# Kernel tuning notes

Measured on AMD Instinct MI355X. Metric: run time of the kernel, lower is better.

The kernel has to match this reference:

```python
import jax, jax.numpy as jnp
import numpy as np

B, NQ, C = 2, 16384, 768
NH, NL, NP = 6, 1, 4
HW = 128
D = C // NH  # 128, deform_ratio = 1.0
EPS = 1e-6


def layernorm(x, g, b):
    m = jnp.mean(x, -1, keepdims=True)
    v = jnp.var(x, -1, keepdims=True)
    return (x - m) * jax.lax.rsqrt(v + EPS) * g + b


def setup_inputs() -> dict:
    key = jax.random.key(0)
    ks = jax.random.split(key, 16)
    n = lambda k, s, sc=1.0: jax.random.normal(k, s, jnp.float32) * sc
    return {
        "query": n(ks[0], (B, NQ, C)),
        "reference_points": jax.random.uniform(ks[1], (B, NQ, NL, 2), jnp.float32),
        "feat": n(ks[2], (B, NQ, C)),
        "spatial_shapes": jnp.array([[HW, HW]], jnp.int32),
        "level_start_index": jnp.array([0], jnp.int32),
        "qn_g": jnp.ones((C,), jnp.float32), "qn_b": jnp.zeros((C,), jnp.float32),
        "fn_g": jnp.ones((C,), jnp.float32), "fn_b": jnp.zeros((C,), jnp.float32),
        "gamma": n(ks[3], (C,), 0.1),
        "W_off": n(ks[4], (C, NH * NL * NP * 2), 0.02), "b_off": n(ks[5], (NH * NL * NP * 2,), 0.5),
        "W_attn": n(ks[6], (C, NH * NL * NP), 0.02), "b_attn": jnp.zeros((NH * NL * NP,), jnp.float32),
        "W_val": n(ks[7], (C, NH * D), 0.02), "b_val": jnp.zeros((NH * D,), jnp.float32),
        "W_out": n(ks[8], (NH * D, C), 0.02), "b_out": jnp.zeros((C,), jnp.float32),
    }


def _ms_deform_attn(q, rp, f, W_off, b_off, W_attn, b_attn, W_val, b_val, W_out, b_out, shapes, starts):
    Bq, Nq, _ = q.shape
    value = (f @ W_val + b_val).reshape(Bq, -1, NH, D)  # (B, Lin, H, D)
    off = (q @ W_off + b_off).reshape(Bq, Nq, NH, NL, NP, 2)
    aw = jax.nn.softmax((q @ W_attn + b_attn).reshape(Bq, Nq, NH, NL * NP), -1)
    aw = aw.reshape(Bq, Nq, NH, NL, NP)
    shapes_f = jnp.asarray(shapes, q.dtype)
    normalizer = jnp.stack([shapes_f[:, 1], shapes_f[:, 0]], -1)  # (NL, 2) = (W, H)
    loc = rp[:, :, None, :, None, :] + off / normalizer[None, None, None, :, None, :]
    out = jnp.zeros((Bq, Nq, NH, D), q.dtype)
    b_idx = jnp.arange(Bq)[:, None, None, None]
    h_idx = jnp.arange(NH)[None, None, :, None]
    for l in range(NL):
        Hl, Wl = int(shapes[l, 0]), int(shapes[l, 1])
        s = int(starts[l])
        v = value[:, s:s + Hl * Wl].reshape(Bq, Hl, Wl, NH, D)
        ll = loc[:, :, :, l]                        # (B, Nq, H, P, 2)
        # grid_sample bilinear, align_corners=False, zero padding
        x = ll[..., 0] * Wl - 0.5
        y = ll[..., 1] * Hl - 0.5
        x0 = jnp.floor(x); y0 = jnp.floor(y)
        x1 = x0 + 1.0;     y1 = y0 + 1.0
        wx1 = x - x0; wx0 = 1.0 - wx1
        wy1 = y - y0; wy0 = 1.0 - wy1
        def corner(xi, yi, w):
            valid = (xi >= 0) & (xi <= Wl - 1) & (yi >= 0) & (yi <= Hl - 1)
            xc = jnp.clip(xi, 0, Wl - 1).astype(jnp.int32)
            yc = jnp.clip(yi, 0, Hl - 1).astype(jnp.int32)
            g = v[b_idx, yc, xc, h_idx]             # (B, Nq, H, P, D)
            return g * (w * valid)[..., None]
        samp = (corner(x0, y0, wx0 * wy0) + corner(x1, y0, wx1 * wy0)
                + corner(x0, y1, wx0 * wy1) + corner(x1, y1, wx1 * wy1))
        out = out + jnp.einsum('bqhpd,bqhp->bqhd', samp, aw[:, :, :, l])
    return out.reshape(Bq, Nq, NH * D) @ W_out + b_out


def reference(query, reference_points, feat, spatial_shapes, level_start_index,
              qn_g, qn_b, fn_g, fn_b, gamma,
              W_off, b_off, W_attn, b_attn, W_val, b_val, W_out, b_out):
    shapes = np.asarray(spatial_shapes)
    starts = np.asarray(level_start_index)
    q = layernorm(query, qn_g, qn_b)
    f = layernorm(feat, fn_g, fn_b)
    attn = _ms_deform_attn(q, reference_points, f, W_off, b_off, W_attn, b_attn,
                           W_val, b_val, W_out, b_out, shapes, starts)
    return query + gamma * attn
```

## Files before the change

kernel.cpp:

```cpp
#include <hip/hip_runtime.h>
#include <stdint.h>

typedef unsigned short u16;
typedef float f32x16 __attribute__((ext_vector_type(16)));
typedef short s16x8 __attribute__((ext_vector_type(8)));

#define K_DIM 768
#define M_ROWS 32768
#define NQ_ 16384
#define HW_ 128

__device__ __forceinline__ float bf2f(u16 u) {
    union { uint32_t u; float f; } c; c.u = ((uint32_t)u) << 16; return c.f;
}
__device__ __forceinline__ u16 f2bf(float f) {
    union { float f; uint32_t u; } c; c.f = f;
    uint32_t u = c.u;
    u += 0x7FFFu + ((u >> 16) & 1);
    return (u16)(u >> 16);
}

__device__ __forceinline__ void gload_lds16(const void* g, void* l) {
    __builtin_amdgcn_global_load_lds((const __attribute__((address_space(1))) void*)g,
                                     (__attribute__((address_space(3))) void*)l, 16, 0, 0);
}

__global__ void prep_all_kernel(const float* __restrict__ Wval, const float* __restrict__ Wout,
                                const float* __restrict__ Woff, const float* __restrict__ Wattn,
                                const float* __restrict__ boff, const float* __restrict__ battn,
                                u16* __restrict__ wv_t, u16* __restrict__ wo_t,
                                u16* __restrict__ woa_t, float* __restrict__ bias) {
    int idx = blockIdx.x * 256 + threadIdx.x;
    const int SZ = 768 * K_DIM;
    if (idx < SZ) {
        int n = idx / K_DIM, k = idx - n * K_DIM;
        wv_t[idx] = f2bf(Wval[(size_t)k * 768 + n]);
    } else if (idx < 2 * SZ) {
        int r = idx - SZ;
        int n = r / K_DIM, k = r - n * K_DIM;
        wo_t[r] = f2bf(Wout[(size_t)k * 768 + n]);
    } else if (idx < 2 * SZ + 128 * K_DIM) {
        int r = idx - 2 * SZ;
        int n = r / K_DIM, k = r - n * K_DIM;
        float v = 0.0f;
        if (n < 48)      v = Woff[(size_t)k * 48 + n];
        else if (n < 72) v = Wattn[(size_t)k * 24 + (n - 48)];
        woa_t[r] = f2bf(v);
        if (r < 128) bias[r] = r < 48 ? boff[r] : (r < 72 ? battn[r - 48] : 0.0f);
    }
}

__global__ __launch_bounds__(256) void ln_kernel(const float* __restrict__ x,
                                                 const float* __restrict__ g,
                                                 const float* __restrict__ b,
                                                 u16* __restrict__ out) {
    const int row = blockIdx.x * 4 + (threadIdx.x >> 6);
    const int lane = threadIdx.x & 63;
    float4 v[3];
    float s = 0.0f, s2 = 0.0f;
#pragma unroll
    for (int j = 0; j < 3; ++j) {
        v[j] = ((const float4*)(x + (size_t)row * K_DIM))[lane + 64 * j];
        s  += v[j].x + v[j].y + v[j].z + v[j].w;
        s2 += v[j].x * v[j].x + v[j].y * v[j].y + v[j].z * v[j].z + v[j].w * v[j].w;
    }
#pragma unroll
    for (int off = 32; off >= 1; off >>= 1) {
        s  += __shfl_xor(s, off);
        s2 += __shfl_xor(s2, off);
    }
    const float mean = s * (1.0f / K_DIM);
    const float var  = s2 * (1.0f / K_DIM) - mean * mean;
    const float inv  = rsqrtf(var + 1e-6f);
#pragma unroll
    for (int j = 0; j < 3; ++j) {
        const float4 gg = ((const float4*)g)[lane + 64 * j];
        const float4 bb = ((const float4*)b)[lane + 64 * j];
        ushort4 o;
        o.x = f2bf((v[j].x - mean) * inv * gg.x + bb.x);
        o.y = f2bf((v[j].y - mean) * inv * gg.y + bb.y);
        o.z = f2bf((v[j].z - mean) * inv * gg.z + bb.z);
        o.w = f2bf((v[j].w - mean) * inv * gg.w + bb.w);
        ((ushort4*)(out + (size_t)row * K_DIM))[lane + 64 * j] = o;
    }
}

#define EP_VAL 0
#define EP_OA 1
#define EP_FINAL 2

template <int EP, int NX, int BN = 128>
__global__ __launch_bounds__(512) void gemm_kernel(
        const u16* __restrict__ A, const u16* __restrict__ Bt,
        const float* __restrict__ bias, void* __restrict__ out, int ld_out,
        const float* __restrict__ query, const float* __restrict__ gamma) {
    constexpr int WN  = (BN >= 128) ? 4 : 2;
    constexpr int WM  = 8 / WN;
    constexpr int MW  = 128 / WM;
    constexpr int MF  = MW / 32;
    constexpr int BCH = BN / 64;
    constexpr int BUF = 16384 + BN * 128;
    constexpr int NWG = NX * (M_ROWS / 128);
    constexpr int CPX = NWG / 8;
    __shared__ __align__(16) char smem[2 * BUF];
    const int lane = threadIdx.x & 63;
    const int wv = threadIdx.x >> 6;
    const int wr = wv / WN, wc = wv % WN;
    const int lr = lane & 31, hi = lane >> 5;
    const int wg  = blockIdx.x;
    const int swz = (wg & 7) * CPX + (wg >> 3);
    const int m0 = (swz / NX) * 128;
    const int n0 = (swz % NX) * BN;

    f32x16 acc[MF] = {};

    const u16* Ab = A + (size_t)m0 * K_DIM;
    const u16* Bb = Bt + (size_t)n0 * K_DIM;

    auto stage = [&](char* buf, int kt) {
#pragma unroll
        for (int c = 0; c < 2; ++c) {
            int chunk = wv * 2 + c;
            int row = chunk * 8 + (lane >> 3);
            int slot = (lane & 7) ^ (row & 7);
            gload_lds16(Ab + (size_t)row * K_DIM + kt + slot * 8, buf + chunk * 1024);
        }
#pragma unroll
        for (int c = 0; c < BCH; ++c) {
            int chunk = wv * BCH + c;
            int row = chunk * 8 + (lane >> 3);
            int slot = (lane & 7) ^ (row & 7);
            gload_lds16(Bb + (size_t)row * K_DIM + kt + slot * 8, buf + 16384 + chunk * 1024);
        }
    };

    stage(smem, 0);
    asm volatile("s_waitcnt vmcnt(0)" ::: "memory");
    __builtin_amdgcn_s_barrier();
    __builtin_amdgcn_sched_barrier(0);

    constexpr int NT = K_DIM / 64;
    int cur = 0;
#pragma unroll 2
    for (int t = 0; t < NT; ++t) {
        const char* rb = smem + cur * BUF;
        if (t + 1 < NT) stage(smem + (cur ^ 1) * BUF, (t + 1) * 64);
#pragma unroll
        for (int kk = 0; kk < 4; ++kk) {
            s16x8 af[MF], bfr;
#pragma unroll
            for (int mi = 0; mi < MF; ++mi) {
                int row = wr * MW + mi * 32 + lr;
                int slot = (kk * 2 + hi) ^ (row & 7);
                af[mi] = *(const s16x8*)(rb + row * 128 + slot * 16);
            }
            {
                int row = wc * 32 + lr;
                int slot = (kk * 2 + hi) ^ (row & 7);
                bfr = *(const s16x8*)(rb + 16384 + row * 128 + slot * 16);
            }
            __builtin_amdgcn_s_setprio(1);
#pragma unroll
            for (int mi = 0; mi < MF; ++mi)
                acc[mi] = __builtin_amdgcn_mfma_f32_32x32x16_bf16(af[mi], bfr, acc[mi], 0, 0, 0);
            __builtin_amdgcn_s_setprio(0);
        }
        asm volatile("s_waitcnt vmcnt(0)" ::: "memory");
        __builtin_amdgcn_s_barrier();
        __builtin_amdgcn_sched_barrier(0);
        cur ^= 1;
    }

    const int col = n0 + wc * 32 + lr;
#pragma unroll
    for (int mi = 0; mi < MF; ++mi) {
#pragma unroll
        for (int reg = 0; reg < 16; ++reg) {
            int row = m0 + wr * MW + mi * 32 + (reg & 3) + 8 * (reg >> 2) + 4 * hi;
            float v = acc[mi][reg] + bias[col];
            if constexpr (EP == EP_VAL) {
                ((u16*)out)[((size_t)(col >> 7) * M_ROWS + row) * 128 + (col & 127)] = f2bf(v);
            } else if constexpr (EP == EP_OA) {
                if (col < 72) {
                    int hh, s;
                    if (col < 48) { hh = col >> 3; s = col & 7; }
                    else          { hh = (col - 48) >> 2; s = 8 + ((col - 48) & 3); }
                    ((float*)out)[((size_t)hh * M_ROWS + row) * 12 + s] = v;
                }
            } else {
                size_t idx = (size_t)row * ld_out + col;
                float qv = __builtin_nontemporal_load(query + idx);
                __builtin_nontemporal_store(qv + gamma[col] * v, (float*)out + idx);
            }
        }
    }
}

__global__ __launch_bounds__(512) void sample_kernel(
        const float* __restrict__ oa2,
        const float* __restrict__ rp,
        const u16* __restrict__ value,
        u16* __restrict__ samp) {
    const int h = blockIdx.x >> 12;
    const int q = __builtin_amdgcn_readfirstlane(
                      ((blockIdx.x & 4095) << 3) + (threadIdx.x >> 6));
    const int lane = threadIdx.x & 63;
    const int b = q >> 14;
    const float* oar = oa2 + ((size_t)h * M_ROWS + q) * 12;

    const int p  = (lane >> 2) & 3;
    const int cn = lane & 3;
    const float lp = oar[8 + p];
    const float e  = __expf(lp);
    float es = e;
    es += __shfl_xor(es, 4);
    es += __shfl_xor(es, 8);
    const float aw = e * __builtin_amdgcn_rcpf(es);

    const float2 offv = *(const float2*)(oar + p * 2);
    const float2 rpv  = *(const float2*)(rp + (size_t)q * 2);
    const float xx = rpv.x * 128.0f + offv.x - 0.5f;
    const float yy = rpv.y * 128.0f + offv.y - 0.5f;
    const float x0 = floorf(xx), y0 = floorf(yy);
    const float fx = xx - x0, fy = yy - y0;
    const float cx = x0 + (float)(cn & 1);
    const float cy = y0 + (float)(cn >> 1);
    const float wx = (cn & 1) ? fx : 1.0f - fx;
    const float wy = (cn >> 1) ? fy : 1.0f - fy;
    const bool valid = (cx >= 0.0f) & (cx <= 127.0f) & (cy >= 0.0f) & (cy <= 127.0f);
    const float w = valid ? aw * wx * wy : 0.0f;
    const int cxi = (int)fminf(fmaxf(cx, 0.0f), 127.0f);
    const int cyi = (int)fminf(fmaxf(cy, 0.0f), 127.0f);
    const int packed = (__float_as_int(w) & 0xffff0000) | (cyi * HW_ + cxi);

    const char* vbs = (const char*)value + ((size_t)h * M_ROWS + (size_t)b * NQ_) * 256;
    float acc0 = 0.0f, acc1 = 0.0f;
#pragma unroll
    for (int c = 0; c < 16; ++c) {
        const int pc = __builtin_amdgcn_readlane(packed, c);
        const float wc = __int_as_float(pc & 0xffff0000);
        const int   oc = (pc & 0x3fff) << 8;
        const uint32_t d = ((const uint32_t*)(vbs + oc))[lane];
        acc0 = fmaf(wc, __int_as_float(d << 16), acc0);
        acc1 = fmaf(wc, __int_as_float(d), acc1);
    }
    ushort2 o; o.x = f2bf(acc0); o.y = f2bf(acc1);
    ((ushort2*)(samp + (size_t)q * K_DIM + h * 128))[lane] = o;
}

extern "C" void kernel_launch(void* const* d_in, const int* in_sizes, int n_in,
                              void* d_out, int out_size, void* d_ws, size_t ws_size,
                              hipStream_t stream) {
    (void)in_sizes; (void)n_in; (void)out_size; (void)ws_size;
    const float* query  = (const float*)d_in[0];
    const float* rp     = (const float*)d_in[1];
    const float* feat   = (const float*)d_in[2];
    const float* qn_g   = (const float*)d_in[5];
    const float* qn_b   = (const float*)d_in[6];
    const float* fn_g   = (const float*)d_in[7];
    const float* fn_b   = (const float*)d_in[8];
    const float* gamma  = (const float*)d_in[9];
    const float* W_off  = (const float*)d_in[10];
    const float* b_off  = (const float*)d_in[11];
    const float* W_attn = (const float*)d_in[12];
    const float* b_attn = (const float*)d_in[13];
    const float* W_val  = (const float*)d_in[14];
    const float* b_val  = (const float*)d_in[15];
    const float* W_out  = (const float*)d_in[16];
    const float* b_out  = (const float*)d_in[17];

    char* ws = (char*)d_ws;
    u16*   ln_buf  = (u16*)  (ws + 0);
    u16*   val_buf = (u16*)  (ws + 50331648);
    float* oa2_buf = (float*)(ws + 100663296);
    u16*   wv_t    = (u16*)  (ws + 117440512);
    u16*   wo_t    = (u16*)  (ws + 118620160);
    u16*   woa_t   = (u16*)  (ws + 119799808);
    float* bias_oa = (float*)(ws + 119996416);
    u16*   samp_buf = ln_buf;

    prep_all_kernel<<<(2 * 768 * 768 + 128 * 768 + 255) / 256, 256, 0, stream>>>(
        W_val, W_out, W_off, W_attn, b_off, b_attn, wv_t, wo_t, woa_t, bias_oa);

    ln_kernel<<<M_ROWS / 4, 256, 0, stream>>>(feat, fn_g, fn_b, ln_buf);

    gemm_kernel<EP_VAL, 6><<<6 * (M_ROWS / 128), 512, 0, stream>>>(ln_buf, wv_t, b_val, val_buf, 768, nullptr, nullptr);

    ln_kernel<<<M_ROWS / 4, 256, 0, stream>>>(query, qn_g, qn_b, ln_buf);

    gemm_kernel<EP_OA, 2, 64><<<2 * (M_ROWS / 128), 512, 0, stream>>>(ln_buf, woa_t, bias_oa, oa2_buf, 0, nullptr, nullptr);

    sample_kernel<<<6 * 4096, 512, 0, stream>>>(oa2_buf, rp, val_buf, samp_buf);

    gemm_kernel<EP_FINAL, 6><<<6 * (M_ROWS / 128), 512, 0, stream>>>(samp_buf, wo_t, b_out, d_out, 768, query, gamma);
}
```

Measured before the change: 232.3 us.

## Tile the weight transpose through LDS and use nontemporal loads/stores

Replaces the strided-read weight transpose for W_val/W_out with a 64x64 LDS-tiled transpose so both global reads and writes are coalesced, and splits the offset/attention weight prep into its own kernel. It also switches LayerNorm input loads, value-GEMM epilogue stores and sampler output stores to nontemporal hints to reduce cache pollution for streaming data. The nontemporal hints may hurt where the written buffers are soon reread (the value buffer by the sampler, the sampled buffer by the final GEMM), and the split adds one kernel launch.

```diff
diff --git a/kernel.cpp b/kernel.cpp
--- a/kernel.cpp
+++ b/kernel.cpp
@@ -3,6 +3,7 @@
 
 typedef unsigned short u16;
 typedef float f32x16 __attribute__((ext_vector_type(16)));
+typedef float f32x4v __attribute__((ext_vector_type(4)));
 typedef short s16x8 __attribute__((ext_vector_type(8)));
 
 #define K_DIM 768
@@ -25,29 +26,35 @@
                                      (__attribute__((address_space(3))) void*)l, 16, 0, 0);
 }
 
-__global__ void prep_all_kernel(const float* __restrict__ Wval, const float* __restrict__ Wout,
-                                const float* __restrict__ Woff, const float* __restrict__ Wattn,
-                                const float* __restrict__ boff, const float* __restrict__ battn,
-                                u16* __restrict__ wv_t, u16* __restrict__ wo_t,
-                                u16* __restrict__ woa_t, float* __restrict__ bias) {
+__global__ __launch_bounds__(256) void prep_tr_kernel(
+        const float* __restrict__ W0, const float* __restrict__ W1,
+        u16* __restrict__ T0, u16* __restrict__ T1) {
+    __shared__ float tile[64][65];
+    const float* W = blockIdx.y ? W1 : W0;
+    u16* T = blockIdx.y ? T1 : T0;
+    const int bi = (blockIdx.x / 12) * 64;
+    const int bj = (blockIdx.x % 12) * 64;
+    const int tx = threadIdx.x & 63, ty = threadIdx.x >> 6;
+#pragma unroll
+    for (int r = 0; r < 64; r += 4)
+        tile[r + ty][tx] = W[(size_t)(bi + r + ty) * 768 + bj + tx];
+    __syncthreads();
+#pragma unroll
+    for (int r = 0; r < 64; r += 4)
+        T[(size_t)(bj + r + ty) * 768 + bi + tx] = f2bf(tile[tx][r + ty]);
+}
+
+__global__ void prep_oa_kernel(const float* __restrict__ Woff, const float* __restrict__ Wattn,
+                               const float* __restrict__ boff, const float* __restrict__ battn,
+                               u16* __restrict__ woa_t, float* __restrict__ bias) {
     int idx = blockIdx.x * 256 + threadIdx.x;
-    const int SZ = 768 * K_DIM;
-    if (idx < SZ) {
-        int n = idx / K_DIM, k = idx - n * K_DIM;
-        wv_t[idx] = f2bf(Wval[(size_t)k * 768 + n]);
-    } else if (idx < 2 * SZ) {
-        int r = idx - SZ;
-        int n = r / K_DIM, k = r - n * K_DIM;
-        wo_t[r] = f2bf(Wout[(size_t)k * 768 + n]);
-    } else if (idx < 2 * SZ + 128 * K_DIM) {
-        int r = idx - 2 * SZ;
-        int n = r / K_DIM, k = r - n * K_DIM;
-        float v = 0.0f;
-        if (n < 48)      v = Woff[(size_t)k * 48 + n];
-        else if (n < 72) v = Wattn[(size_t)k * 24 + (n - 48)];
-        woa_t[r] = f2bf(v);
-        if (r < 128) bias[r] = r < 48 ? boff[r] : (r < 72 ? battn[r - 48] : 0.0f);
-    }
+    if (idx >= 128 * K_DIM) return;
+    int n = idx / K_DIM, k = idx - n * K_DIM;
+    float v = 0.0f;
+    if (n < 48)      v = Woff[(size_t)k * 48 + n];
+    else if (n < 72) v = Wattn[(size_t)k * 24 + (n - 48)];
+    woa_t[idx] = f2bf(v);
+    if (idx < 128) bias[idx] = idx < 48 ? boff[idx] : (idx < 72 ? battn[idx - 48] : 0.0f);
 }
 
 __global__ __launch_bounds__(256) void ln_kernel(const float* __restrict__ x,
@@ -56,11 +63,12 @@
                                                  u16* __restrict__ out) {
     const int row = blockIdx.x * 4 + (threadIdx.x >> 6);
     const int lane = threadIdx.x & 63;
-    float4 v[3];
+    const f32x4v* xp = (const f32x4v*)(x + (size_t)row * K_DIM);
+    f32x4v v[3];
     float s = 0.0f, s2 = 0.0f;
 #pragma unroll
     for (int j = 0; j < 3; ++j) {
-        v[j] = ((const float4*)(x + (size_t)row * K_DIM))[lane + 64 * j];
+        v[j] = __builtin_nontemporal_load(xp + lane + 64 * j);
         s  += v[j].x + v[j].y + v[j].z + v[j].w;
         s2 += v[j].x * v[j].x + v[j].y * v[j].y + v[j].z * v[j].z + v[j].w * v[j].w;
     }
@@ -179,7 +187,8 @@
             int row = m0 + wr * MW + mi * 32 + (reg & 3) + 8 * (reg >> 2) + 4 * hi;
             float v = acc[mi][reg] + bias[col];
             if constexpr (EP == EP_VAL) {
-                ((u16*)out)[((size_t)(col >> 7) * M_ROWS + row) * 128 + (col & 127)] = f2bf(v);
+                __builtin_nontemporal_store(f2bf(v),
+                    (u16*)out + ((size_t)(col >> 7) * M_ROWS + row) * 128 + (col & 127));
             } else if constexpr (EP == EP_OA) {
                 if (col < 72) {
                     int hh, s;
@@ -244,8 +253,9 @@
         acc0 = fmaf(wc, __int_as_float(d << 16), acc0);
         acc1 = fmaf(wc, __int_as_float(d), acc1);
     }
-    ushort2 o; o.x = f2bf(acc0); o.y = f2bf(acc1);
-    ((ushort2*)(samp + (size_t)q * K_DIM + h * 128))[lane] = o;
+    const uint32_t ov = (uint32_t)f2bf(acc0) | ((uint32_t)f2bf(acc1) << 16);
+    __builtin_nontemporal_store(ov,
+        (uint32_t*)(samp + (size_t)q * K_DIM + h * 128) + lane);
 }
 
 extern "C" void kernel_launch(void* const* d_in, const int* in_sizes, int n_in,
@@ -279,8 +289,9 @@
     float* bias_oa = (float*)(ws + 119996416);
     u16*   samp_buf = ln_buf;
 
-    prep_all_kernel<<<(2 * 768 * 768 + 128 * 768 + 255) / 256, 256, 0, stream>>>(
-        W_val, W_out, W_off, W_attn, b_off, b_attn, wv_t, wo_t, woa_t, bias_oa);
+    prep_tr_kernel<<<dim3(144, 2), 256, 0, stream>>>(W_val, W_out, wv_t, wo_t);
+    prep_oa_kernel<<<(128 * 768 + 255) / 256, 256, 0, stream>>>(
+        W_off, W_attn, b_off, b_attn, woa_t, bias_oa);
 
     ln_kernel<<<M_ROWS / 4, 256, 0, stream>>>(feat, fn_g, fn_b, ln_buf);
 
```

Measured after the change: 248.3 us. +6.9%, slower.
